# Kernel tuning notes

Measured on AMD Instinct MI355X. Metric: run time of the kernel, lower is better.

The kernel has to match this reference:

```python
import jax, jax.numpy as jnp
import numpy as np

N = 30000
DEG = 16
E_RAND = N * DEG
E = E_RAND + N  # with self loops appended
T = 2
F_IN, H1, OUT = 128, 128, 64
NBSZ = 15
AGG = 0.8
NEG_SLOPE = 0.2


def setup_inputs() -> dict:
    key = jax.random.key(0)
    ks = jax.random.split(key, 10)
    x_all = jax.random.normal(ks[0], (T, N, F_IN), dtype=jnp.float32)
    # edges per snapshot: random edges + self loops (mirrors remove_self_loops + add_self_loops)
    loops = jnp.arange(N, dtype=jnp.int32)
    eis = []
    for t in range(T):
        src = jax.random.randint(jax.random.fold_in(ks[1], t), (E_RAND,), 0, N, dtype=jnp.int32)
        dst = jax.random.randint(jax.random.fold_in(ks[2], t), (E_RAND,), 0, N, dtype=jnp.int32)
        eis.append(jnp.stack([jnp.concatenate([src, loops]), jnp.concatenate([dst, loops])]))
    edge_index_all = jnp.stack(eis)  # [T, 2, E]
    def glorot(k, shape):
        fan = shape[0] + shape[-1]
        s = jnp.sqrt(6.0 / fan)
        return jax.random.uniform(k, shape, jnp.float32, -s, s)
    W1 = glorot(ks[3], (F_IN, 2 * H1))
    att1 = glorot(ks[4], (1, 1, 4 * H1))   # [1, heads=1, 2*out_neurons]
    b1 = jnp.zeros((2 * H1,), jnp.float32)
    W2 = glorot(ks[5], (H1, 2 * OUT))
    att2 = glorot(ks[6], (1, 1, 4 * OUT))
    b2 = jnp.zeros((2 * OUT,), jnp.float32)
    return {"x_all": x_all, "edge_index_all": edge_index_all,
            "W1": W1, "att1": att1, "b1": b1, "W2": W2, "att2": att2, "b2": b2}


def _conv(x, edge_index, W, att, b, C):
    """One DGIBConv (heads=1, Bernoulli distribution, diag reparam, eval mode).
    Returns (node_out [N,C], ixz scalar, structure_kl scalar)."""
    h = x @ W                                    # [N, 2C]
    src, dst = edge_index[0], edge_index[1]
    x_j = h[src]                                 # [E, 2C] per-edge gather (source)
    x_i = h[dst]                                 # [E, 2C] target
    a = att[0, 0]                                # [4C]
    logits = jnp.sum(x_i * a[:2 * C], -1) + jnp.sum(x_j * a[2 * C:], -1)  # [E]
    logits = jax.nn.leaky_relu(logits, NEG_SLOPE)
    # Bernoulli branch: softmax of ones over segments == 1/deg(dst)
    deg = jax.ops.segment_sum(jnp.ones_like(logits), dst, num_segments=N)  # [N]
    norm = 1.0 / deg[dst]
    p = jnp.clip(jax.nn.sigmoid(logits), 0.01, 0.99)  # posterior Bernoulli probs
    alpha = p * norm
    aggr = jax.ops.segment_sum(x_j * alpha[:, None], dst, num_segments=N) + b  # [N, 2C]
    # diag reparam: mean || std-logit split; Gaussian prior N(0, I)
    mu = aggr[:, :C]
    std = jax.nn.softplus(aggr[:, C:]) + 1e-10
    kl = -jnp.log(std) + 0.5 * (std * std + mu * mu) - 0.5  # KL(N(mu,std)||N(0,1)) per dim
    ixz = jnp.mean(jnp.sum(kl, -1))
    # structure KL: Bernoulli(p) || Bernoulli(logits = 1/nbsz)
    q = jax.nn.sigmoid(jnp.float32(1.0 / NBSZ))
    skl = jnp.mean(p * jnp.log(p / q) + (1.0 - p) * jnp.log((1.0 - p) / (1.0 - q)))
    return mu, ixz, skl


def _layer(x_list, edge_index_all, W, att, b, C):
    """Temporal DGIBConv.forward: per-snapshot conv + weighted temporal fusion."""
    outs, ixzs, skls = [], [], []
    for t in range(T):
        out, ixz, skl = _conv(x_list[t], edge_index_all[t], W, att, b, C)
        if t > 0:
            w = jax.nn.sigmoid(jnp.arange(t, dtype=jnp.float32))[:, None, None]  # [t,1,1]
            prev = jnp.stack(outs[:t])                                           # [t,N,C]
            out = jnp.sum(w * prev, 0) / t * AGG + out * (1.0 - AGG)
        outs.append(out)
        ixzs.append(ixz)
        skls.append(skl)
    return outs, jnp.mean(jnp.stack(ixzs)), jnp.mean(jnp.stack(skls))


def reference(x_all, edge_index_all, W1, att1, b1, W2, att2, b2):
    xs = [x_all[t] for t in range(T)]
    h1, ixz1, skl1 = _layer(xs, edge_index_all, W1, att1, b1, H1)
    h1 = [jax.nn.relu(h) for h in h1]  # with_relu=True, eval -> dropout is identity
    h2, ixz2, skl2 = _layer(h1, edge_index_all, W2, att2, b2, OUT)
    out = jnp.stack(h2)                # [T, N, OUT]
    ixz_mean = (ixz1 + ixz2) / 2.0
    skl_mean = (skl1 + skl2) / 2.0
    return out, ixz_mean, skl_mean
```

## Files before the change

### kernel.cpp

```cpp
#include <hip/hip_runtime.h>
#include <hip/hip_bf16.h>
#include <hip/hip_fp8.h>

#define N_NODES 30000
#define N_EDGES 510000
#define K_DIM   128
#define ABLK    7500

typedef short bf16x8 __attribute__((ext_vector_type(8)));
typedef float f32x4  __attribute__((ext_vector_type(4)));
typedef float f32x2  __attribute__((ext_vector_type(2)));

__device__ __forceinline__ unsigned short f2bf(float f) {
  __hip_bfloat16 h = __float2bfloat16(f);
  return *(unsigned short*)&h;
}
__device__ __forceinline__ unsigned char f2fp8(float f) {
  __hip_fp8_e4m3 q(f);
  return (unsigned char)q.__x;
}
__device__ __forceinline__ float fp82f(unsigned char u) {
  __hip_fp8_e4m3 q;
  q.__x = (__hip_fp8_storage_t)u;
  return (float)q;
}

__global__ void transpose_w_kernel(const float* __restrict__ W1, unsigned short* __restrict__ Wt1,
                                   const float* __restrict__ W2, unsigned short* __restrict__ Wt2) {
  int i = blockIdx.x * blockDim.x + threadIdx.x;
  if (i < 128 * 256) {
    int k = i >> 8, m = i & 255;
    Wt1[m * 128 + k] = f2bf(W1[i]);
  } else if (i < 128 * 256 + 128 * 128) {
    int j = i - 128 * 256;
    int k = j >> 7, m = j & 127;
    Wt2[m * 128 + k] = f2bf(W2[j]);
  }
}

__global__ void deg_kernel(const int* __restrict__ ei, int* __restrict__ deg0,
                           int* __restrict__ deg1, int e) {
  int i = blockIdx.x * blockDim.x + threadIdx.x;
  if (i < 2 * e) {
    int t = i >= e ? 1 : 0;
    int j = i - t * e;
    int d = ei[(size_t)t * 2 * e + e + j];
    atomicAdd(&(t ? deg1 : deg0)[d], 1);
  }
}

__global__ __launch_bounds__(1024) void scan_kernel(const int* __restrict__ deg0, int* __restrict__ off0, int* __restrict__ cur0,
                                                    const int* __restrict__ deg1, int* __restrict__ off1, int* __restrict__ cur1,
                                                    int n) {
  const int* deg = blockIdx.x ? deg1 : deg0;
  int* off = blockIdx.x ? off1 : off0;
  int* cur = blockIdx.x ? cur1 : cur0;
  const int CHUNK = 30;
  __shared__ int wsum[16];
  int tid = threadIdx.x;
  int base = tid * CHUNK;
  int sum = 0;
  for (int i = 0; i < CHUNK; i++)
    if (base + i < n) sum += deg[base + i];
  int lane = tid & 63, wid = tid >> 6;
  int incl = sum;
#pragma unroll
  for (int o = 1; o < 64; o <<= 1) {
    int v = __shfl_up(incl, o);
    if (lane >= o) incl += v;
  }
  if (lane == 63) wsum[wid] = incl;
  __syncthreads();
  if (tid == 0) {
    int run = 0;
    for (int w = 0; w < 16; w++) { int v = wsum[w]; wsum[w] = run; run += v; }
  }
  __syncthreads();
  int run = incl - sum + wsum[wid];
  for (int i = 0; i < CHUNK; i++) {
    if (base + i < n) {
      off[base + i] = run;
      cur[base + i] = run;
      run += deg[base + i];
    }
  }
}

__global__ void scatter_kernel(const int* __restrict__ ei,
                               int* __restrict__ cur0, int* __restrict__ cur1,
                               int* __restrict__ csr0, int* __restrict__ csr1, int e) {
  int i = blockIdx.x * blockDim.x + threadIdx.x;
  if (i < 2 * e) {
    int t = i >= e ? 1 : 0;
    int j = i - t * e;
    int s = ei[(size_t)t * 2 * e + j];
    int d = ei[(size_t)t * 2 * e + e + j];
    int* cur = t ? cur1 : cur0;
    int* csr = t ? csr1 : csr0;
    int p = atomicAdd(&cur[d], 1);
    csr[p] = s;
  }
}

template<int M, bool F32IN>
__global__ __launch_bounds__(256) void gemm_kernel(const void* __restrict__ X0v,
                                                   const void* __restrict__ X1v,
                                                   const short* __restrict__ Wt,
                                                   unsigned char* __restrict__ H0,
                                                   unsigned char* __restrict__ H1,
                                                   const float* __restrict__ att,
                                                   float* __restrict__ si0, float* __restrict__ si1,
                                                   float* __restrict__ sj0, float* __restrict__ sj1,
                                                   int nrows) {
  int t = blockIdx.y;
  const void* Xv = t ? X1v : X0v;
  unsigned char* Hf8 = t ? H1 : H0;
  float* s_i = t ? si1 : si0;
  float* s_j = t ? sj1 : sj0;

  int wave = blockIdx.x * 4 + (threadIdx.x >> 6);
  int lane = threadIdx.x & 63;
  if (wave * 16 >= nrows) return;
  int m16 = lane & 15, quad = lane >> 4;

  bf16x8 a[4];
  size_t arow = (size_t)(wave * 16 + m16) * K_DIM + quad * 8;
  if constexpr (F32IN) {
    const float* X = (const float*)Xv;
#pragma unroll
    for (int kc = 0; kc < 4; kc++) {
      f32x4 lo = *(const f32x4*)(X + arow + kc * 32);
      f32x4 hi = *(const f32x4*)(X + arow + kc * 32 + 4);
#pragma unroll
      for (int j = 0; j < 4; j++) {
        ((unsigned short*)&a[kc])[j]     = f2bf(lo[j]);
        ((unsigned short*)&a[kc])[4 + j] = f2bf(hi[j]);
      }
    }
  } else {
    const short* X = (const short*)Xv;
#pragma unroll
    for (int kc = 0; kc < 4; kc++) a[kc] = *(const bf16x8*)(X + arow + kc * 32);
  }

  float sip[4] = {0.f, 0.f, 0.f, 0.f}, sjp[4] = {0.f, 0.f, 0.f, 0.f};
#pragma unroll
  for (int nt = 0; nt < M / 16; nt++) {
    f32x4 acc = {0.f, 0.f, 0.f, 0.f};
    size_t brow = (size_t)(nt * 16 + m16) * K_DIM + quad * 8;
#pragma unroll
    for (int kc = 0; kc < 4; kc++) {
      bf16x8 b = *(const bf16x8*)(Wt + brow + kc * 32);
      acc = __builtin_amdgcn_mfma_f32_16x16x32_bf16(a[kc], b, acc, 0, 0, 0);
    }
    int col = nt * 16 + m16;
    float aA = att[col], aB = att[M + col];
#pragma unroll
    for (int r = 0; r < 4; r++) {
      int row = wave * 16 + quad * 4 + r;
      Hf8[(size_t)row * M + col] = f2fp8(acc[r]);
      sip[r] += acc[r] * aA;
      sjp[r] += acc[r] * aB;
    }
  }
#pragma unroll
  for (int o = 1; o < 16; o <<= 1) {
#pragma unroll
    for (int r = 0; r < 4; r++) {
      sip[r] += __shfl_xor(sip[r], o);
      sjp[r] += __shfl_xor(sjp[r], o);
    }
  }
  if (m16 == 0) {
#pragma unroll
    for (int r = 0; r < 4; r++) {
      int row = wave * 16 + quad * 4 + r;
      s_i[row] = sip[r];
      s_j[row] = sjp[r];
    }
  }
}

template<int M>
__global__ __launch_bounds__(256) void aggr_kernel(const unsigned char* __restrict__ H0,
                                                   const unsigned char* __restrict__ H1,
                                                   const int* __restrict__ csr0, const int* __restrict__ csr1,
                                                   const int* __restrict__ off0, const int* __restrict__ off1,
                                                   const int* __restrict__ deg0, const int* __restrict__ deg1,
                                                   const float* __restrict__ si0, const float* __restrict__ si1,
                                                   const float* __restrict__ sj0, const float* __restrict__ sj1,
                                                   const float* __restrict__ bias,
                                                   float* __restrict__ mu0, float* __restrict__ mu1,
                                                   f32x2* __restrict__ partials,
                                                   int n) {
  constexpr int C = M / 2;
  constexpr int V = M / 64;
  constexpr int U = 16;

  int t = blockIdx.y;
  const unsigned char* Hf8 = t ? H1 : H0;
  const int* csr = t ? csr1 : csr0;
  const int* off = t ? off1 : off0;
  const int* deg = t ? deg1 : deg0;
  const float* s_i = t ? si1 : si0;
  const float* s_j = t ? sj1 : sj0;
  float* mu = t ? mu1 : mu0;

  __shared__ float red_i[4], red_s[4];
  int wid = threadIdx.x >> 6, lane = threadIdx.x & 63;
  int wave = blockIdx.x * 4 + wid;
  float ixz = 0.f, skl = 0.f;

  if (wave < n) {
    int d     = __builtin_amdgcn_readfirstlane(deg[wave]);
    int start = __builtin_amdgcn_readfirstlane(off[wave]);
    float si  = s_i[wave];
    float norm = 1.0f / (float)d;
    int c0 = lane * V;
    const float q   = 1.0f / (1.0f + __expf(-(1.0f / 15.0f)));
    const float lq  = __logf(q);
    const float l1q = __logf(1.0f - q);

    float acc[V];
#pragma unroll
    for (int k = 0; k < V; k++) acc[k] = 0.f;

    for (int e0 = 0; e0 < d; e0 += U) {
      int idxs[U];
#pragma unroll
      for (int u = 0; u < U; u++) {
        int ee = e0 + u;
        int ap = start + (ee < d ? ee : 0);
        idxs[u] = __builtin_amdgcn_readfirstlane(csr[ap]);
      }
      unsigned int hv[U];
#pragma unroll
      for (int u = 0; u < U; u++) {
        if constexpr (V == 4)
          hv[u] = *(const unsigned int*)(Hf8 + (size_t)idxs[u] * M + c0);
        else
          hv[u] = (unsigned int)*(const unsigned short*)(Hf8 + (size_t)idxs[u] * M + c0);
      }
      float ws[U];
#pragma unroll
      for (int u = 0; u < U; u++) {
        bool valid = (e0 + u) < d;
        float lg = si + s_j[idxs[u]];
        lg = lg > 0.f ? lg : 0.2f * lg;
        float p = 1.0f / (1.0f + __expf(-lg));
        p = fminf(fmaxf(p, 0.01f), 0.99f);
        if (valid)
          skl += p * (__logf(p) - lq) + (1.0f - p) * (__logf(1.0f - p) - l1q);
        ws[u] = valid ? p : 0.f;
      }
#pragma unroll
      for (int u = 0; u < U; u++) {
#pragma unroll
        for (int k = 0; k < V; k++)
          acc[k] += ws[u] * fp82f((unsigned char)(hv[u] >> (8 * k)));
      }
    }

    if (c0 < C) {
#pragma unroll
      for (int k = 0; k < V; k++) {
        float a = acc[k] * norm + bias[c0 + k];
        acc[k] = a;
        ixz += 0.5f * a * a - 0.5f;
      }
      if constexpr (V == 4)
        *(f32x4*)(mu + (size_t)wave * C + c0) = *(f32x4*)acc;
      else
        *(f32x2*)(mu + (size_t)wave * C + c0) = *(f32x2*)acc;
    } else {
#pragma unroll
      for (int k = 0; k < V; k++) {
        float a = acc[k] * norm + bias[c0 + k];
        float sp = (a > 20.f) ? a : log1pf(__expf(a));
        sp += 1e-10f;
        ixz += -__logf(sp) + 0.5f * sp * sp;
      }
    }
  }
#pragma unroll
  for (int o = 32; o > 0; o >>= 1) ixz += __shfl_xor(ixz, o);
  if (lane == 0) { red_i[wid] = ixz; red_s[wid] = skl; }
  __syncthreads();
  if (threadIdx.x == 0) {
    f32x2 pr;
    pr[0] = red_i[0] + red_i[1] + red_i[2] + red_i[3];
    pr[1] = red_s[0] + red_s[1] + red_s[2] + red_s[3];
    partials[t * ABLK + blockIdx.x] = pr;
  }
}

__global__ void fuse1_kernel(const float* __restrict__ mu0, const float* __restrict__ mu1,
                             __hip_bfloat16* __restrict__ x0, __hip_bfloat16* __restrict__ x1, int n) {
  int i = blockIdx.x * blockDim.x + threadIdx.x;
  if (i < n) {
    float m0 = mu0[i], m1 = mu1[i];
    x0[i] = __float2bfloat16(fmaxf(m0, 0.f));
    x1[i] = __float2bfloat16(fmaxf(0.4f * m0 + 0.2f * m1, 0.f));
  }
}

__global__ void fuse2_kernel(const float* __restrict__ mu0, const float* __restrict__ mu1,
                             float* __restrict__ out, int n) {
  int i = blockIdx.x * blockDim.x + threadIdx.x;
  if (i < n) {
    float m0 = mu0[i], m1 = mu1[i];
    out[i] = m0;
    out[n + i] = 0.4f * m0 + 0.2f * m1;
  }
}

__global__ __launch_bounds__(1024) void reduce_kernel(const f32x2* __restrict__ p1,
                                                      const f32x2* __restrict__ p2,
                                                      float* __restrict__ out2) {
  __shared__ float ri[16], rs[16];
  float ixz = 0.f, skl = 0.f;
  for (int i = threadIdx.x; i < 2 * ABLK; i += 1024) {
    f32x2 a = p1[i], b = p2[i];
    ixz += a[0] + b[0];
    skl += a[1] + b[1];
  }
  int lane = threadIdx.x & 63, wid = threadIdx.x >> 6;
#pragma unroll
  for (int o = 32; o > 0; o >>= 1) {
    ixz += __shfl_xor(ixz, o);
    skl += __shfl_xor(skl, o);
  }
  if (lane == 0) { ri[wid] = ixz; rs[wid] = skl; }
  __syncthreads();
  if (threadIdx.x == 0) {
    float si = 0.f, ss = 0.f;
    for (int w = 0; w < 16; w++) { si += ri[w]; ss += rs[w]; }
    out2[0] = si / (4.0f * (float)N_NODES);
    out2[1] = ss / (4.0f * (float)N_EDGES);
  }
}

extern "C" void kernel_launch(void* const* d_in, const int* in_sizes, int n_in,
                              void* d_out, int out_size, void* d_ws, size_t ws_size,
                              hipStream_t stream) {
  const float* x_all = (const float*)d_in[0];
  const int* ei      = (const int*)d_in[1];
  const float* W1    = (const float*)d_in[2];
  const float* att1  = (const float*)d_in[3];
  const float* b1    = (const float*)d_in[4];
  const float* W2    = (const float*)d_in[5];
  const float* att2  = (const float*)d_in[6];
  const float* b2    = (const float*)d_in[7];
  float* out         = (float*)d_out;

  char* ws = (char*)d_ws;
  size_t off = 0;
  auto alloc = [&](size_t bytes) {
    char* p = ws + off;
    off = (off + bytes + 255) & ~(size_t)255;
    return p;
  };
  unsigned short* wt1  = (unsigned short*)alloc(256 * 128 * sizeof(short));
  unsigned short* wt2  = (unsigned short*)alloc(128 * 128 * sizeof(short));
  unsigned char* hf8_0 = (unsigned char*)alloc((size_t)N_NODES * 256);
  unsigned char* hf8_1 = (unsigned char*)alloc((size_t)N_NODES * 256);
  float* si0   = (float*)alloc(N_NODES * sizeof(float));
  float* si1   = (float*)alloc(N_NODES * sizeof(float));
  float* sj0   = (float*)alloc(N_NODES * sizeof(float));
  float* sj1   = (float*)alloc(N_NODES * sizeof(float));
  float* mu1_0 = (float*)alloc((size_t)N_NODES * 128 * sizeof(float));
  float* mu1_1 = (float*)alloc((size_t)N_NODES * 128 * sizeof(float));
  __hip_bfloat16* x2_0 = (__hip_bfloat16*)alloc((size_t)N_NODES * 128 * sizeof(short));
  __hip_bfloat16* x2_1 = (__hip_bfloat16*)alloc((size_t)N_NODES * 128 * sizeof(short));
  float* mu2_0 = mu1_0;
  float* mu2_1 = mu1_0 + (size_t)N_NODES * 64;
  int* degp[2]  = {(int*)alloc(N_NODES * 4), (int*)alloc(N_NODES * 4)};
  int* offp[2]  = {(int*)alloc(N_NODES * 4), (int*)alloc(N_NODES * 4)};
  int* curp[2]  = {(int*)alloc(N_NODES * 4), (int*)alloc(N_NODES * 4)};
  int* csrp[2]  = {(int*)alloc(N_EDGES * 4), (int*)alloc(N_EDGES * 4)};
  f32x2* part1  = (f32x2*)alloc(2 * ABLK * sizeof(f32x2));
  f32x2* part2  = (f32x2*)alloc(2 * ABLK * sizeof(f32x2));

  hipMemsetAsync(degp[0], 0, N_NODES * 4, stream);
  hipMemsetAsync(degp[1], 0, N_NODES * 4, stream);

  transpose_w_kernel<<<192, 256, 0, stream>>>(W1, wt1, W2, wt2);

  deg_kernel<<<(2 * N_EDGES + 255) / 256, 256, 0, stream>>>(ei, degp[0], degp[1], N_EDGES);
  scan_kernel<<<2, 1024, 0, stream>>>(degp[0], offp[0], curp[0], degp[1], offp[1], curp[1], N_NODES);
  scatter_kernel<<<(2 * N_EDGES + 255) / 256, 256, 0, stream>>>(ei, curp[0], curp[1],
                                                                csrp[0], csrp[1], N_EDGES);

  dim3 ggrid(469, 2), agrid(ABLK, 2);

  const float* x0 = x_all;
  const float* x1 = x_all + (size_t)N_NODES * K_DIM;
  gemm_kernel<256, true><<<ggrid, 256, 0, stream>>>(x0, x1, (const short*)wt1, hf8_0, hf8_1,
                                                    att1, si0, si1, sj0, sj1, N_NODES);
  aggr_kernel<256><<<agrid, 256, 0, stream>>>(hf8_0, hf8_1, csrp[0], csrp[1], offp[0], offp[1],
                                              degp[0], degp[1], si0, si1, sj0, sj1, b1,
                                              mu1_0, mu1_1, part1, N_NODES);
  fuse1_kernel<<<(N_NODES * 128 + 255) / 256, 256, 0, stream>>>(mu1_0, mu1_1, x2_0, x2_1, N_NODES * 128);

  gemm_kernel<128, false><<<ggrid, 256, 0, stream>>>(x2_0, x2_1, (const short*)wt2, hf8_0, hf8_1,
                                                     att2, si0, si1, sj0, sj1, N_NODES);
  aggr_kernel<128><<<agrid, 256, 0, stream>>>(hf8_0, hf8_1, csrp[0], csrp[1], offp[0], offp[1],
                                              degp[0], degp[1], si0, si1, sj0, sj1, b2,
                                              mu2_0, mu2_1, part2, N_NODES);
  fuse2_kernel<<<(N_NODES * 64 + 255) / 256, 256, 0, stream>>>(mu2_0, mu2_1, out, N_NODES * 64);
  reduce_kernel<<<1, 1024, 0, stream>>>(part1, part2, out + (size_t)2 * N_NODES * 64);
}
```

Measured before the change: 645.0 us.

## Restructure GAT aggregation: lane-parallel edge weights, 8-byte fp8 gathers, packed conversion

The aggregation kernel now has each lane compute the attention weight and skl term for a different edge, instead of every lane redundantly computing all 16. Lanes are split into groups that each handle different edges, loading 8 fp8 features per lane with one 8-byte load and converting them with the packed fp8-to-f32 builtin. A cross-group shuffle reduction then combines the partial accumulators. skl is now reduced across lanes because it is computed per lane. The trade-off is extra shuffles for broadcasting indices and weights and for the final reduction.

```diff
diff --git a/kernel.cpp b/kernel.cpp
--- a/kernel.cpp
+++ b/kernel.cpp
@@ -10,6 +10,7 @@
 typedef short bf16x8 __attribute__((ext_vector_type(8)));
 typedef float f32x4  __attribute__((ext_vector_type(4)));
 typedef float f32x2  __attribute__((ext_vector_type(2)));
+typedef unsigned int u32x2 __attribute__((ext_vector_type(2)));
 
 __device__ __forceinline__ unsigned short f2bf(float f) {
   __hip_bfloat16 h = __float2bfloat16(f);
@@ -18,11 +19,6 @@
 __device__ __forceinline__ unsigned char f2fp8(float f) {
   __hip_fp8_e4m3 q(f);
   return (unsigned char)q.__x;
-}
-__device__ __forceinline__ float fp82f(unsigned char u) {
-  __hip_fp8_e4m3 q;
-  q.__x = (__hip_fp8_storage_t)u;
-  return (float)q;
 }
 
 __global__ void transpose_w_kernel(const float* __restrict__ W1, unsigned short* __restrict__ Wt1,
@@ -194,8 +190,11 @@
                                                    f32x2* __restrict__ partials,
                                                    int n) {
   constexpr int C = M / 2;
-  constexpr int V = M / 64;
-  constexpr int U = 16;
+  constexpr int LPR = M / 8;
+  constexpr int LOG2LPR = (M == 256) ? 5 : 4;
+  constexpr int EPL = 64 / LPR;
+  constexpr int NL = 4;
+  constexpr int U = NL * EPL;
 
   int t = blockIdx.y;
   const unsigned char* Hf8 = t ? H1 : H0;
@@ -216,74 +215,107 @@
     int start = __builtin_amdgcn_readfirstlane(off[wave]);
     float si  = s_i[wave];
     float norm = 1.0f / (float)d;
-    int c0 = lane * V;
+    int sub = lane & (LPR - 1);
+    int g   = lane >> LOG2LPR;
+    int c0  = sub * 8;
     const float q   = 1.0f / (1.0f + __expf(-(1.0f / 15.0f)));
     const float lq  = __logf(q);
     const float l1q = __logf(1.0f - q);
 
-    float acc[V];
-#pragma unroll
-    for (int k = 0; k < V; k++) acc[k] = 0.f;
+    float acc[8];
+#pragma unroll
+    for (int k = 0; k < 8; k++) acc[k] = 0.f;
 
     for (int e0 = 0; e0 < d; e0 += U) {
-      int idxs[U];
-#pragma unroll
-      for (int u = 0; u < U; u++) {
-        int ee = e0 + u;
-        int ap = start + (ee < d ? ee : 0);
-        idxs[u] = __builtin_amdgcn_readfirstlane(csr[ap]);
+      int ee = e0 + lane;
+      bool val = (lane < U) && (ee < d);
+      int ap = start + (val ? ee : (d - 1));
+      int idxl = csr[ap];
+      float sjl = s_j[idxl];
+      float lg = si + sjl;
+      lg = lg > 0.f ? lg : 0.2f * lg;
+      float p = 1.0f / (1.0f + __expf(-lg));
+      p = fminf(fmaxf(p, 0.01f), 0.99f);
+      float wl = val ? p : 0.f;
+      if (val)
+        skl += p * (__logf(p) - lq) + (1.0f - p) * (__logf(1.0f - p) - l1q);
+
+      u32x2 hv[NL];
+      float wsel[NL];
+#pragma unroll
+      for (int l = 0; l < NL; l++) {
+        int idx; float wv_;
+        if constexpr (EPL == 2) {
+          int i0 = __shfl(idxl, l * 2), i1 = __shfl(idxl, l * 2 + 1);
+          float w0 = __shfl(wl, l * 2), w1 = __shfl(wl, l * 2 + 1);
+          idx = g ? i1 : i0;
+          wv_ = g ? w1 : w0;
+        } else {
+          int i0 = __shfl(idxl, l * 4),     i1 = __shfl(idxl, l * 4 + 1);
+          int i2 = __shfl(idxl, l * 4 + 2), i3 = __shfl(idxl, l * 4 + 3);
+          float w0 = __shfl(wl, l * 4),     w1 = __shfl(wl, l * 4 + 1);
+          float w2 = __shfl(wl, l * 4 + 2), w3 = __shfl(wl, l * 4 + 3);
+          int ia = (g & 1) ? i1 : i0, ib = (g & 1) ? i3 : i2;
+          idx = (g & 2) ? ib : ia;
+          float fa = (g & 1) ? w1 : w0, fb = (g & 1) ? w3 : w2;
+          wv_ = (g & 2) ? fb : fa;
+        }
+        wsel[l] = wv_;
+        hv[l] = *(const u32x2*)(Hf8 + (size_t)idx * M + c0);
       }
-      unsigned int hv[U];
-#pragma unroll
-      for (int u = 0; u < U; u++) {
-        if constexpr (V == 4)
-          hv[u] = *(const unsigned int*)(Hf8 + (size_t)idxs[u] * M + c0);
-        else
-          hv[u] = (unsigned int)*(const unsigned short*)(Hf8 + (size_t)idxs[u] * M + c0);
+#pragma unroll
+      for (int l = 0; l < NL; l++) {
+        f32x2 d0 = __builtin_amdgcn_cvt_pk_f32_fp8((int)hv[l][0], false);
+        f32x2 d1 = __builtin_amdgcn_cvt_pk_f32_fp8((int)hv[l][0], true);
+        f32x2 d2 = __builtin_amdgcn_cvt_pk_f32_fp8((int)hv[l][1], false);
+        f32x2 d3 = __builtin_amdgcn_cvt_pk_f32_fp8((int)hv[l][1], true);
+        float wv_ = wsel[l];
+        acc[0] += wv_ * d0[0]; acc[1] += wv_ * d0[1];
+        acc[2] += wv_ * d1[0]; acc[3] += wv_ * d1[1];
+        acc[4] += wv_ * d2[0]; acc[5] += wv_ * d2[1];
+        acc[6] += wv_ * d3[0]; acc[7] += wv_ * d3[1];
       }
-      float ws[U];
-#pragma unroll
-      for (int u = 0; u < U; u++) {
-        bool valid = (e0 + u) < d;
-        float lg = si + s_j[idxs[u]];
-        lg = lg > 0.f ? lg : 0.2f * lg;
-        float p = 1.0f / (1.0f + __expf(-lg));
-        p = fminf(fmaxf(p, 0.01f), 0.99f);
-        if (valid)
-          skl += p * (__logf(p) - lq) + (1.0f - p) * (__logf(1.0f - p) - l1q);
-        ws[u] = valid ? p : 0.f;
+    }
+
+#pragma unroll
+    for (int o = LPR; o < 64; o <<= 1) {
+#pragma unroll
+      for (int k = 0; k < 8; k++) acc[k] += __shfl_xor(acc[k], o);
+    }
+
+    if (lane < LPR) {
+      if (c0 < C) {
+        f32x4 m0, m1;
+#pragma unroll
+        for (int k = 0; k < 4; k++) {
+          float a = acc[k] * norm + bias[c0 + k];
+          m0[k] = a;
+          ixz += 0.5f * a * a - 0.5f;
+        }
+#pragma unroll
+        for (int k = 0; k < 4; k++) {
+          float a = acc[4 + k] * norm + bias[c0 + 4 + k];
+          m1[k] = a;
+          ixz += 0.5f * a * a - 0.5f;
+        }
+        *(f32x4*)(mu + (size_t)wave * C + c0) = m0;
+        *(f32x4*)(mu + (size_t)wave * C + c0 + 4) = m1;
+      } else {
+#pragma unroll
+        for (int k = 0; k < 8; k++) {
+          float a = acc[k] * norm + bias[c0 + k];
+          float sp = (a > 20.f) ? a : log1pf(__expf(a));
+          sp += 1e-10f;
+          ixz += -__logf(sp) + 0.5f * sp * sp;
+        }
       }
-#pragma unroll
-      for (int u = 0; u < U; u++) {
-#pragma unroll
-        for (int k = 0; k < V; k++)
-          acc[k] += ws[u] * fp82f((unsigned char)(hv[u] >> (8 * k)));
-      }
-    }
-
-    if (c0 < C) {
-#pragma unroll
-      for (int k = 0; k < V; k++) {
-        float a = acc[k] * norm + bias[c0 + k];
-        acc[k] = a;
-        ixz += 0.5f * a * a - 0.5f;
-      }
-      if constexpr (V == 4)
-        *(f32x4*)(mu + (size_t)wave * C + c0) = *(f32x4*)acc;
-      else
-        *(f32x2*)(mu + (size_t)wave * C + c0) = *(f32x2*)acc;
-    } else {
-#pragma unroll
-      for (int k = 0; k < V; k++) {
-        float a = acc[k] * norm + bias[c0 + k];
-        float sp = (a > 20.f) ? a : log1pf(__expf(a));
-        sp += 1e-10f;
-        ixz += -__logf(sp) + 0.5f * sp * sp;
-      }
-    }
-  }
-#pragma unroll
-  for (int o = 32; o > 0; o >>= 1) ixz += __shfl_xor(ixz, o);
+    }
+  }
+#pragma unroll
+  for (int o = 32; o > 0; o >>= 1) {
+    ixz += __shfl_xor(ixz, o);
+    skl += __shfl_xor(skl, o);
+  }
   if (lane == 0) { red_i[wid] = ixz; red_s[wid] = skl; }
   __syncthreads();
   if (threadIdx.x == 0) {
```

Result: faster. 591.9 us (-8.2%).
